# Kernel tuning notes

Measured on AMD Instinct MI355X. Metric: run time of the kernel, lower is better.

The kernel has to match this reference:

```python
import jax, jax.numpy as jnp
import numpy as np

B, T, C = 4, 2048, 1024
N_HEAD = 16
HEAD_DIM = C // N_HEAD


def setup_inputs() -> dict:
    key = jax.random.key(0)
    k1, k2, k3 = jax.random.split(key, 3)
    x = jax.random.normal(k1, (B, T, C), dtype=jnp.float32)
    # torch Linear(n_embd, 3*n_embd, bias=False): weight [out,in]; store transposed [in,out]
    w_qkv = jax.random.normal(k2, (C, 3 * C), dtype=jnp.float32) * (1.0 / np.sqrt(C))
    w_proj = jax.random.normal(k3, (C, C), dtype=jnp.float32) * (1.0 / np.sqrt(C))
    return {"x": x, "w_qkv": w_qkv, "w_proj": w_proj}


def reference(x, w_qkv, w_proj):
    Bb, Tt, Cc = x.shape
    qkv = x @ w_qkv  # [B,T,3C]
    q, k, v = jnp.split(qkv, 3, axis=2)
    # [B,T,H,D] -> [B,H,T,D]
    def heads(t):
        return t.reshape(Bb, Tt, N_HEAD, HEAD_DIM).transpose(0, 2, 1, 3)
    q, k, v = heads(q), heads(k), heads(v)
    att = jnp.einsum("bhqd,bhkd->bhqk", q, k) / jnp.sqrt(jnp.float32(HEAD_DIM))
    causal = jnp.tril(jnp.ones((Tt, Tt), dtype=bool))
    att = jnp.where(causal, att, -jnp.inf)
    att = jax.nn.softmax(att, axis=-1)
    y = jnp.einsum("bhqk,bhkd->bhqd", att, v)  # [B,H,T,D]
    y = y.transpose(0, 2, 1, 3).reshape(Bb, Tt, Cc)
    return y @ w_proj
```

## Files before the change

kernel.cpp:

```cpp
#include <hip/hip_runtime.h>
#include <hip/hip_bf16.h>

typedef unsigned short u16;
typedef __bf16 bf16x8 __attribute__((ext_vector_type(8)));
typedef float f32x4 __attribute__((ext_vector_type(4)));
typedef float f32x16 __attribute__((ext_vector_type(16)));
typedef unsigned short u16x8 __attribute__((ext_vector_type(8)));
typedef unsigned short u16x4 __attribute__((ext_vector_type(4)));
typedef unsigned int u32x4 __attribute__((ext_vector_type(4)));

__device__ __forceinline__ u16 f2bf(float f) {
  unsigned u = __builtin_bit_cast(unsigned, f);
  u += 0x7FFFu + ((u >> 16) & 1u);
  return (u16)(u >> 16);
}

__device__ __forceinline__ unsigned cvt_pk_bf16(float lo, float hi_) {
  unsigned r;
  asm("v_cvt_pk_bf16_f32 %0, %1, %2" : "=v"(r) : "v"(lo), "v"(hi_));
  return r;
}

#define GLD16(gp, lp)                                                          \
  __builtin_amdgcn_global_load_lds(                                            \
      (const __attribute__((address_space(1))) void*)(gp),                     \
      (__attribute__((address_space(3))) void*)(lp), 16, 0, 0)


__global__ __launch_bounds__(256) void cast_f32_bf16(
    const float* __restrict__ in, u16* __restrict__ out, int n4) {
  int i = blockIdx.x * 256 + threadIdx.x;
  if (i >= n4) return;
  float4 v = ((const float4*)in)[i];
  u16x4 o = {f2bf(v.x), f2bf(v.y), f2bf(v.z), f2bf(v.w)};
  *(u16x4*)(out + (size_t)i * 4) = o;
}

__global__ __launch_bounds__(256) void transpose_cast(
    const float* __restrict__ in, u16* __restrict__ out, int R, int C) {
  __shared__ float t[32][33];
  int c0 = blockIdx.x * 32, r0 = blockIdx.y * 32;
  int tx = threadIdx.x, ty = threadIdx.y;
#pragma unroll
  for (int k = 0; k < 4; ++k)
    t[ty + 8 * k][tx] = in[(size_t)(r0 + ty + 8 * k) * C + c0 + tx];
  __syncthreads();
#pragma unroll
  for (int k = 0; k < 4; ++k)
    out[(size_t)(c0 + ty + 8 * k) * R + r0 + tx] = f2bf(t[tx][ty + 8 * k]);
}


template <int EPI>
__global__ __launch_bounds__(256) void gemm_bt(
    const u16* __restrict__ A, const u16* __restrict__ Bt, int K,
    u16* __restrict__ Qd, u16* __restrict__ Kd, u16* __restrict__ Vd,
    float* __restrict__ Od, int N) {
  __shared__ u16 As[128 * 64];
  __shared__ u16 Bs[128 * 64];
  int tid = threadIdx.x;
  int l = tid & 63, w = tid >> 6;
  int wr = w >> 1, wc = w & 1;
  int lr = l & 15, lg = l >> 4;
  int m0 = blockIdx.y * 128, n0 = blockIdx.x * 128;

  f32x4 acc[4][4];
  f32x4 z4 = {0.f, 0.f, 0.f, 0.f};
#pragma unroll
  for (int mi = 0; mi < 4; ++mi)
#pragma unroll
    for (int ni = 0; ni < 4; ++ni) acc[mi][ni] = z4;

  for (int kt = 0; kt < K; kt += 64) {
#pragma unroll
    for (int it = 0; it < 4; ++it) {
      int q = it * 256 + tid;
      int r = q >> 3, s = q & 7;
      int sw = (s ^ (r & 7)) << 3;
      GLD16(A + (size_t)(m0 + r) * K + kt + sw, As + it * 2048 + w * 512);
      GLD16(Bt + (size_t)(n0 + r) * K + kt + sw, Bs + it * 2048 + w * 512);
    }
    __syncthreads();

#pragma unroll
    for (int ks2 = 0; ks2 < 2; ++ks2) {
      bf16x8 af[4], bfv[4];
#pragma unroll
      for (int mi = 0; mi < 4; ++mi) {
        int row = wr * 64 + mi * 16 + lr;
        af[mi] = *(const bf16x8*)&As[row * 64 + (((ks2 * 4 + lg) ^ (row & 7)) << 3)];
      }
#pragma unroll
      for (int ni = 0; ni < 4; ++ni) {
        int col = wc * 64 + ni * 16 + lr;
        bfv[ni] = *(const bf16x8*)&Bs[col * 64 + (((ks2 * 4 + lg) ^ (col & 7)) << 3)];
      }
#pragma unroll
      for (int mi = 0; mi < 4; ++mi)
#pragma unroll
        for (int ni = 0; ni < 4; ++ni)
          acc[mi][ni] = __builtin_amdgcn_mfma_f32_16x16x32_bf16(
              af[mi], bfv[ni], acc[mi][ni], 0, 0, 0);
    }
    __syncthreads();
  }

  if (EPI == 0) {
    int s_blk = n0 >> 10;
    u16* dst = (s_blk == 0) ? Qd : ((s_blk == 1) ? Kd : Vd);
#pragma unroll
    for (int mi = 0; mi < 4; ++mi)
#pragma unroll
      for (int ni = 0; ni < 4; ++ni)
#pragma unroll
        for (int i = 0; i < 4; ++i) {
          int m = m0 + wr * 64 + mi * 16 + lg * 4 + i;
          int n = n0 + wc * 64 + ni * 16 + lr;
          int b = m >> 11, t = m & 2047;
          int c = n & 1023, h = c >> 6, d = c & 63;
          dst[((size_t)(b * 16 + h) * 2048 + t) * 64 + d] = f2bf(acc[mi][ni][i]);
        }
  } else {
#pragma unroll
    for (int mi = 0; mi < 4; ++mi)
#pragma unroll
      for (int ni = 0; ni < 4; ++ni)
#pragma unroll
        for (int i = 0; i < 4; ++i) {
          int m = m0 + wr * 64 + mi * 16 + lg * 4 + i;
          int n = n0 + wc * 64 + ni * 16 + lr;
          Od[(size_t)m * N + n] = acc[mi][ni][i];
        }
  }
}


__global__ __launch_bounds__(128, 3) void attn_fwd(
    const u16* __restrict__ Qg, const u16* __restrict__ Kg,
    const u16* __restrict__ Vg, u16* __restrict__ Yg) {
  __shared__ u16 Ks[2][64 * 64];
  __shared__ u16 Vt[64 * 64];

  int tid = threadIdx.x;
  int l = tid & 63, w = tid >> 6;
  int l31 = l & 31, hi = l >> 5, l7 = l & 7;
  int bid = blockIdx.x;
  int qt = 31 - (bid >> 6);
  int bh = bid & 63;
  const u16* Qb = Qg + (size_t)bh * 131072;
  const u16* Kb = Kg + (size_t)bh * 131072;
  const u16* Vb = Vg + (size_t)bh * 131072;
  int b = bh >> 4, h = bh & 15;

  int t8 = tid >> 3, dq = tid & 7;
  int q0w = qt * 64 + w * 32;
  int jn = qt;

  bf16x8 qreg[4];
#pragma unroll
  for (int ds = 0; ds < 4; ++ds)
    qreg[ds] =
        *(const bf16x8*)(Qb + (size_t)(q0w + l31) * 64 + ds * 16 + hi * 8);

  f32x16 o_acc[2];
#pragma unroll
  for (int dt = 0; dt < 2; ++dt)
#pragma unroll
    for (int r = 0; r < 16; ++r) o_acc[dt][r] = 0.f;
  float m_run = -3e38f, l_run = 0.f;

  u16x8 va[2], vb[2];
#pragma unroll
  for (int it = 0; it < 4; ++it) {
    int r = it * 16 + t8;
    GLD16(Kb + (size_t)r * 64 + ((dq ^ (r & 7)) << 3),
          &Ks[0][it * 1024 + w * 512]);
  }
#pragma unroll
  for (int it = 0; it < 2; ++it) {
    int rr = it * 16 + t8;
    va[it] = *(const u16x8*)(Vb + (size_t)(2 * rr) * 64 + dq * 8);
    vb[it] = *(const u16x8*)(Vb + (size_t)(2 * rr + 1) * 64 + dq * 8);
  }

  for (int j = 0; j <= jn; ++j) {
    int kv0 = j * 64;
    const u16* ksb = Ks[j & 1];
#pragma unroll
    for (int it = 0; it < 2; ++it) {
      int rr = it * 16 + t8;
      int rr2 = (rr & ~6) | ((rr & 2) << 1) | ((rr & 4) >> 1);
#pragma unroll
      for (int jj = 0; jj < 8; ++jj) {
        int d = dq * 8 + jj;
        unsigned wv = (unsigned)va[it][jj] | ((unsigned)vb[it][jj] << 16);
        *(unsigned*)(Vt + d * 64 + (((rr2 >> 2) ^ jj ^ dq) << 3) +
                     ((rr2 & 3) << 1)) = wv;
      }
    }
    __syncthreads();

    if (j < jn) {
      int kv1 = kv0 + 64;
#pragma unroll
      for (int it = 0; it < 4; ++it) {
        int r = it * 16 + t8;
        GLD16(Kb + (size_t)(kv1 + r) * 64 + ((dq ^ (r & 7)) << 3),
              &Ks[(j + 1) & 1][it * 1024 + w * 512]);
      }
#pragma unroll
      for (int it = 0; it < 2; ++it) {
        int rr = it * 16 + t8;
        va[it] = *(const u16x8*)(Vb + (size_t)(kv1 + 2 * rr) * 64 + dq * 8);
        vb[it] = *(const u16x8*)(Vb + (size_t)(kv1 + 2 * rr + 1) * 64 + dq * 8);
      }
    }

    {
      int qg = q0w + l31;
      bf16x8 kf[2][4];
#pragma unroll
      for (int kt = 0; kt < 2; ++kt)
#pragma unroll
        for (int ds = 0; ds < 4; ++ds)
          kf[kt][ds] = *(const bf16x8*)&ksb[(32 * kt + l31) * 64 +
                                            (((2 * ds + hi) ^ l7) << 3)];
      f32x16 sa[2];
      __builtin_amdgcn_s_setprio(1);
#pragma unroll
      for (int kt = 0; kt < 2; ++kt) {
        f32x16 acc;
#pragma unroll
        for (int r = 0; r < 16; ++r) acc[r] = 0.f;
#pragma unroll
        for (int ds = 0; ds < 4; ++ds)
          acc = __builtin_amdgcn_mfma_f32_32x32x16_bf16(kf[kt][ds], qreg[ds],
                                                        acc, 0, 0, 0);
        sa[kt] = acc;
      }
      __builtin_amdgcn_s_setprio(0);

      float mloc = -3e38f;
      if (kv0 + 63 > q0w) {
#pragma unroll
        for (int kt = 0; kt < 2; ++kt)
#pragma unroll
          for (int r = 0; r < 16; ++r) {
            int kg = kv0 + kt * 32 + ((r & 3) + 8 * (r >> 2) + 4 * hi);
            float v = sa[kt][r];
            v = (kg <= qg) ? v : -8e30f;
            sa[kt][r] = v;
            mloc = fmaxf(mloc, v);
          }
      } else {
#pragma unroll
        for (int kt = 0; kt < 2; ++kt)
#pragma unroll
          for (int r = 0; r < 16; ++r) mloc = fmaxf(mloc, sa[kt][r]);
      }
      float mx = fmaxf(mloc, __shfl_xor(mloc, 32)) * 0.125f;
      if (!__all(mx <= m_run + 8.f)) {
        float mn = fmaxf(m_run, mx);
        float fsc = __expf(m_run - mn);
        m_run = mn;
        l_run *= fsc;
#pragma unroll
        for (int r = 0; r < 16; ++r) {
          float fv = __shfl(fsc, (r & 3) + 8 * (r >> 2) + 4 * hi + 32 * hi);
          o_acc[0][r] *= fv;
          o_acc[1][r] *= fv;
        }
      }
      float mm = m_run * 1.44269504f;
      float lloc = 0.f;
#pragma unroll
      for (int kt = 0; kt < 2; ++kt)
#pragma unroll
        for (int r = 0; r < 16; ++r) {
          float p = exp2f(__builtin_fmaf(sa[kt][r], 0.18033688f, -mm));
          sa[kt][r] = p;
          lloc += p;
        }
      l_run += lloc;
      unsigned pk0[8], pk1[8];
#pragma unroll
      for (int m = 0; m < 8; ++m) {
        pk0[m] = cvt_pk_bf16(sa[0][2 * m], sa[0][2 * m + 1]);
        pk1[m] = cvt_pk_bf16(sa[1][2 * m], sa[1][2 * m + 1]);
      }
      bf16x8 vf[2][4];
#pragma unroll
      for (int dt = 0; dt < 2; ++dt)
#pragma unroll
        for (int ks = 0; ks < 4; ++ks) {
          int d = 32 * dt + l31;
          int ch = ((2 * ks + hi) ^ (d & 7) ^ ((d >> 3) & 7)) & 7;
          vf[dt][ks] = *(const bf16x8*)&Vt[d * 64 + (ch << 3)];
        }
#pragma unroll
      for (int ks = 0; ks < 4; ++ks) {
        int c0 = 4 * (ks & 1);
        u32x4 fa;
        fa.x = (ks < 2) ? pk0[c0] : pk1[c0];
        fa.y = (ks < 2) ? pk0[c0 + 1] : pk1[c0 + 1];
        fa.z = (ks < 2) ? pk0[c0 + 2] : pk1[c0 + 2];
        fa.w = (ks < 2) ? pk0[c0 + 3] : pk1[c0 + 3];
        bf16x8 paf = __builtin_bit_cast(bf16x8, fa);
        __builtin_amdgcn_s_setprio(1);
#pragma unroll
        for (int dt = 0; dt < 2; ++dt)
          o_acc[dt] = __builtin_amdgcn_mfma_f32_32x32x16_bf16(
              paf, vf[dt][ks], o_acc[dt], 0, 0, 0);
        __builtin_amdgcn_s_setprio(0);
      }
    }
    __builtin_amdgcn_sched_barrier(0);
    __builtin_amdgcn_s_barrier();
    __builtin_amdgcn_sched_barrier(0);
  }

  l_run += __shfl_xor(l_run, 32);

#pragma unroll
  for (int r = 0; r < 16; ++r) {
    int crow = (r & 3) + 8 * (r >> 2) + 4 * hi;
    float li = __shfl(l_run, crow + 32 * hi);
    float inv = 1.f / li;
    int q = q0w + crow;
#pragma unroll
    for (int dt = 0; dt < 2; ++dt) {
      float y = o_acc[dt][r] * inv;
      Yg[(size_t)(b * 2048 + q) * 1024 + h * 64 + dt * 32 + l31] = f2bf(y);
    }
  }
}


extern "C" void kernel_launch(void* const* d_in, const int* in_sizes, int n_in,
                              void* d_out, int out_size, void* d_ws, size_t ws_size,
                              hipStream_t stream) {
  const float* x = (const float*)d_in[0];
  const float* w_qkv = (const float*)d_in[1];
  const float* w_proj = (const float*)d_in[2];
  float* out = (float*)d_out;
  u16* ws = (u16*)d_ws;

  u16* xb = ws;
  u16* wq = xb + 8388608;
  u16* wp = wq + 3145728;
  u16* Qb = wp + 1048576;
  u16* Kb = Qb + 8388608;
  u16* Vb = Kb + 8388608;
  u16* Yb = xb;

  cast_f32_bf16<<<8192, 256, 0, stream>>>(x, xb, 2097152);
  transpose_cast<<<dim3(96, 32), dim3(32, 8), 0, stream>>>(w_qkv, wq, 1024, 3072);
  transpose_cast<<<dim3(32, 32), dim3(32, 8), 0, stream>>>(w_proj, wp, 1024, 1024);
  gemm_bt<0><<<dim3(24, 64), 256, 0, stream>>>(xb, wq, 1024, Qb, Kb, Vb, nullptr, 3072);
  attn_fwd<<<2048, 128, 0, stream>>>(Qb, Kb, Vb, Yb);
  gemm_bt<1><<<dim3(8, 64), 256, 0, stream>>>(Yb, wp, 1024, nullptr, nullptr, nullptr, out, 1024);
}
```

Measured before the change: 174.3 us.

## Load K fragments directly from global and double-buffer transposed V in LDS

Removes the LDS staging buffer for K: each wave now reads its K MFMA fragments straight from global memory (L2/L1) rather than through async global-to-LDS loads. The freed LDS is used to double-buffer the transposed V tile, so only one barrier per iteration is needed instead of two. Occupancy hint rises from 3 to 4 blocks per CU. The cost is global-load latency sitting directly in front of the QK MFMAs, with no prefetch to hide it.

```diff
diff --git a/kernel.cpp b/kernel.cpp
--- a/kernel.cpp
+++ b/kernel.cpp
@@ -135,15 +135,14 @@
 }
 
 
-__global__ __launch_bounds__(128, 3) void attn_fwd(
+__global__ __launch_bounds__(128, 4) void attn_fwd(
     const u16* __restrict__ Qg, const u16* __restrict__ Kg,
     const u16* __restrict__ Vg, u16* __restrict__ Yg) {
-  __shared__ u16 Ks[2][64 * 64];
-  __shared__ u16 Vt[64 * 64];
+  __shared__ u16 Vt[2][64 * 64];
 
   int tid = threadIdx.x;
   int l = tid & 63, w = tid >> 6;
-  int l31 = l & 31, hi = l >> 5, l7 = l & 7;
+  int l31 = l & 31, hi = l >> 5;
   int bid = blockIdx.x;
   int qt = 31 - (bid >> 6);
   int bh = bid & 63;
@@ -171,12 +170,6 @@
 
   u16x8 va[2], vb[2];
 #pragma unroll
-  for (int it = 0; it < 4; ++it) {
-    int r = it * 16 + t8;
-    GLD16(Kb + (size_t)r * 64 + ((dq ^ (r & 7)) << 3),
-          &Ks[0][it * 1024 + w * 512]);
-  }
-#pragma unroll
   for (int it = 0; it < 2; ++it) {
     int rr = it * 16 + t8;
     va[it] = *(const u16x8*)(Vb + (size_t)(2 * rr) * 64 + dq * 8);
@@ -185,7 +178,7 @@
 
   for (int j = 0; j <= jn; ++j) {
     int kv0 = j * 64;
-    const u16* ksb = Ks[j & 1];
+    u16* vtp = Vt[j & 1];
 #pragma unroll
     for (int it = 0; it < 2; ++it) {
       int rr = it * 16 + t8;
@@ -194,20 +187,12 @@
       for (int jj = 0; jj < 8; ++jj) {
         int d = dq * 8 + jj;
         unsigned wv = (unsigned)va[it][jj] | ((unsigned)vb[it][jj] << 16);
-        *(unsigned*)(Vt + d * 64 + (((rr2 >> 2) ^ jj ^ dq) << 3) +
+        *(unsigned*)(vtp + d * 64 + (((rr2 >> 2) ^ jj ^ dq) << 3) +
                      ((rr2 & 3) << 1)) = wv;
       }
     }
-    __syncthreads();
-
     if (j < jn) {
       int kv1 = kv0 + 64;
-#pragma unroll
-      for (int it = 0; it < 4; ++it) {
-        int r = it * 16 + t8;
-        GLD16(Kb + (size_t)(kv1 + r) * 64 + ((dq ^ (r & 7)) << 3),
-              &Ks[(j + 1) & 1][it * 1024 + w * 512]);
-      }
 #pragma unroll
       for (int it = 0; it < 2; ++it) {
         int rr = it * 16 + t8;
@@ -215,6 +200,10 @@
         vb[it] = *(const u16x8*)(Vb + (size_t)(kv1 + 2 * rr + 1) * 64 + dq * 8);
       }
     }
+    __builtin_amdgcn_sched_barrier(0);
+    asm volatile("s_waitcnt lgkmcnt(0)" ::: "memory");
+    __builtin_amdgcn_s_barrier();
+    __builtin_amdgcn_sched_barrier(0);
 
     {
       int qg = q0w + l31;
@@ -223,8 +212,9 @@
       for (int kt = 0; kt < 2; ++kt)
 #pragma unroll
         for (int ds = 0; ds < 4; ++ds)
-          kf[kt][ds] = *(const bf16x8*)&ksb[(32 * kt + l31) * 64 +
-                                            (((2 * ds + hi) ^ l7) << 3)];
+          kf[kt][ds] = *(const bf16x8*)(Kb +
+                                        (size_t)(kv0 + 32 * kt + l31) * 64 +
+                                        ds * 16 + hi * 8);
       f32x16 sa[2];
       __builtin_amdgcn_s_setprio(1);
 #pragma unroll
@@ -295,7 +285,7 @@
         for (int ks = 0; ks < 4; ++ks) {
           int d = 32 * dt + l31;
           int ch = ((2 * ks + hi) ^ (d & 7) ^ ((d >> 3) & 7)) & 7;
-          vf[dt][ks] = *(const bf16x8*)&Vt[d * 64 + (ch << 3)];
+          vf[dt][ks] = *(const bf16x8*)&vtp[d * 64 + (ch << 3)];
         }
 #pragma unroll
       for (int ks = 0; ks < 4; ++ks) {
@@ -314,9 +304,6 @@
         __builtin_amdgcn_s_setprio(0);
       }
     }
-    __builtin_amdgcn_sched_barrier(0);
-    __builtin_amdgcn_s_barrier();
-    __builtin_amdgcn_sched_barrier(0);
   }
 
   l_run += __shfl_xor(l_run, 32);
```

Measured after the change: 246.8 us. 41.6% more time.
